# Optimization experiments

Hardware: AMD Instinct MI355X
Metric: run time of the kernel (lower is better)

Reference implementation:

```python
import jax, jax.numpy as jnp
import numpy as np

N1 = 512
N2 = 512
N = N1 + N2
NEG_SLOPE = 0.2


def _build_edges(n1, n2):
    # inside: fully connected within each set, both directions
    s1, d1 = np.triu_indices(n1, 1)
    s2, d2 = np.triu_indices(n2, 1)
    is_ = np.concatenate([s1, s2 + n1])
    id_ = np.concatenate([d1, d2 + n1])
    inside = np.stack([np.concatenate([is_, id_]), np.concatenate([id_, is_])])
    # cross: fully connected bipartite, both directions
    cs = np.repeat(np.arange(n1), n2)
    cd = np.tile(np.arange(n1, n1 + n2), n1)
    cross = np.stack([np.concatenate([cs, cd]), np.concatenate([cd, cs])])
    # PyG GATConv default add_self_loops=True
    loops = np.arange(n1 + n2)
    self_e = np.stack([loops, loops])
    inside = np.concatenate([inside, self_e], axis=1)
    cross = np.concatenate([cross, self_e], axis=1)
    return inside.astype(np.int32), cross.astype(np.int32)


def setup_inputs() -> dict:
    key = jax.random.key(0)
    ks = jax.random.split(key, 12)
    inside_edge, cross_edge = _build_edges(N1, N2)
    s = 0.1
    return {
        'desc1': jax.random.normal(ks[0], (N1, 128), jnp.float32),
        'desc2': jax.random.normal(ks[1], (N2, 128), jnp.float32),
        'W1': jax.random.normal(ks[2], (128, 128), jnp.float32) * s,
        'a_src1': jax.random.normal(ks[3], (128, 1), jnp.float32) * s,
        'a_dst1': jax.random.normal(ks[4], (128, 1), jnp.float32) * s,
        'b1': jnp.zeros((128,), jnp.float32),
        'W2': jax.random.normal(ks[5], (128, 128), jnp.float32) * s,
        'a_src2': jax.random.normal(ks[6], (1, 128), jnp.float32) * s,
        'a_dst2': jax.random.normal(ks[7], (1, 128), jnp.float32) * s,
        'b2': jnp.zeros((128,), jnp.float32),
        'inside_edge': jnp.asarray(inside_edge),
        'cross_edge': jnp.asarray(cross_edge),
    }


def gat_conv(x, edge_index, W, a_src, a_dst, bias, heads, out_ch, concat):
    # x: [N, F_in]; edge_index: [2, E] (self-loops already included)
    n = x.shape[0]
    src, dst = edge_index[0], edge_index[1]
    h = (x @ W).reshape(n, heads, out_ch)                 # [N, H, C]
    a_s = jnp.sum(h * a_src, axis=-1)                     # [N, H]
    a_d = jnp.sum(h * a_dst, axis=-1)                     # [N, H]
    e = jax.nn.leaky_relu(a_s[src] + a_d[dst], NEG_SLOPE)  # [E, H]
    # segment (scatter) softmax over incoming edges of each dst node
    m = jax.ops.segment_max(e, dst, num_segments=n)
    ex = jnp.exp(e - m[dst])
    denom = jax.ops.segment_sum(ex, dst, num_segments=n)
    alpha = ex / (denom[dst] + 1e-16)                     # [E, H]
    out = jax.ops.segment_sum(alpha[:, :, None] * h[src], dst, num_segments=n)  # [N, H, C]
    out = out.reshape(n, heads * out_ch) if concat else out.mean(axis=1)
    return out + bias


def reference(desc1, desc2, W1, a_src1, a_dst1, b1, W2, a_src2, a_dst2, b2, inside_edge, cross_edge):
    x = jnp.concatenate([desc1, desc2], axis=0)  # [N, 128]
    for _ in range(2):
        x = jax.nn.elu(gat_conv(x, inside_edge, W1, a_src1, a_dst1, b1, 128, 1, True))
        x = jax.nn.elu(gat_conv(x, cross_edge, W1, a_src1, a_dst1, b1, 128, 1, True))
    x = gat_conv(x, cross_edge, W2, a_src2, a_dst2, b2, 1, 128, False)  # [N, 128]
    return x
```

## Files before the change

kernel.cpp:

```cpp
#include <hip/hip_runtime.h>
#include <hip/hip_bf16.h>


typedef __hip_bfloat16 bf16;

__device__ __forceinline__ float b2f(bf16 x) { return __bfloat162float(x); }

__device__ __forceinline__ int detect_bf16(const void* desc1) {
  const unsigned* u = (const unsigned*)desc1;
  int hits = 0;
#pragma unroll 8
  for (int i = 0; i < 256; ++i) {
    unsigned e = (u[i] >> 7) & 0xFFu;
    hits += (e >= 100u && e <= 140u) ? 1 : 0;
  }
  return hits >= 200 ? 1 : 0;
}

__device__ __forceinline__ float load_in(const void* p, int i, int bf) {
  return bf ? b2f(((const bf16*)p)[i]) : ((const float*)p)[i];
}

__global__ __launch_bounds__(256) void prep_kernel(
    const void* __restrict__ desc1, const void* __restrict__ desc2,
    const void* __restrict__ W1,   const void* __restrict__ as1,
    const void* __restrict__ ad1,  const void* __restrict__ b1,
    const void* __restrict__ W2,   const void* __restrict__ as2,
    const void* __restrict__ ad2,  const void* __restrict__ b2,
    float* __restrict__ xt, float* __restrict__ W1t, float* __restrict__ W2f,
    float* __restrict__ vecs, int* __restrict__ flag) {
  const int bf = detect_bf16(desc1);
  if (blockIdx.x == 0 && threadIdx.x == 0) *flag = bf;
  const int total = 131072 + 16384 + 16384 + 6 * 128;
  for (int idx = blockIdx.x * blockDim.x + threadIdx.x; idx < total;
       idx += gridDim.x * blockDim.x) {
    if (idx < 131072) {
      int n = idx & 1023, c = idx >> 10;
      float v = (n < 512) ? load_in(desc1, n * 128 + c, bf)
                          : load_in(desc2, (n - 512) * 128 + c, bf);
      xt[((c >> 2) * 1024 + n) * 4 + (c & 3)] = v;
    } else if (idx < 147456) {
      int i = idx - 131072, hd = i >> 7, k = i & 127;
      W1t[i] = load_in(W1, k * 128 + hd, bf);
    } else if (idx < 163840) {
      W2f[idx - 147456] = load_in(W2, idx - 147456, bf);
    } else {
      int i = idx - 163840, o = i & 127;
      float v;
      if      (i < 128) v = load_in(as1, o, bf);
      else if (i < 256) v = load_in(ad1, o, bf);
      else if (i < 384) v = load_in(b1, o, bf);
      else if (i < 512) v = load_in(as2, o, bf);
      else if (i < 640) v = load_in(ad2, o, bf);
      else              v = load_in(b2, o, bf);
      vecs[i] = v;
    }
  }
}

__global__ __launch_bounds__(256, 2) void gemm_kernel(
    const float* __restrict__ xt_in, const float* __restrict__ W1t,
    float* __restrict__ Ht) {
  __shared__ float wcol[128];
  const int tid = threadIdx.x;
  const int hd = blockIdx.x & 127;
  const int chunk = blockIdx.x >> 7;
  const int node = chunk * 256 + tid;
  if (tid < 32) ((float4*)wcol)[tid] = ((const float4*)(W1t + hd * 128))[tid];
  __syncthreads();
  const float4* x4 = (const float4*)xt_in;
  float acc0 = 0.f, acc1 = 0.f;
  for (int cc = 0; cc < 32; cc += 8) {
    float4 xs[8];
#pragma unroll
    for (int u = 0; u < 8; ++u) xs[u] = x4[(cc + u) * 1024 + node];
#pragma unroll
    for (int u = 0; u < 8; ++u) {
      const int k = (cc + u) * 4;
      acc0 = fmaf(xs[u].x, wcol[k],     acc0);
      acc1 = fmaf(xs[u].y, wcol[k + 1], acc1);
      acc0 = fmaf(xs[u].z, wcol[k + 2], acc0);
      acc1 = fmaf(xs[u].w, wcol[k + 3], acc1);
    }
  }
  Ht[hd * 1024 + node] = acc0 + acc1;
}

template <int CROSS>
__global__ __launch_bounds__(512, 2) void attn_kernel(
    const float* __restrict__ Ht, float* __restrict__ xt_out,
    const float* __restrict__ vecs) {
  __shared__ float    sS[512];
  __shared__ float    sH[512];
  __shared__ unsigned hA[512];
  __shared__ unsigned ISb[512];
  __shared__ unsigned binNext[512];
  __shared__ float2   PRE[512];
  __shared__ float2   SUF[512];
  __shared__ float    red[16];
  __shared__ unsigned wTot[8];
  __shared__ float2   preTot[8];
  __shared__ float2   sufTot[8];

  const int tid  = threadIdx.x;
  const int lane = tid & 63;
  const int wave = tid >> 6;
  const int hd   = blockIdx.x & 127;
  const int S    = blockIdx.x >> 7;
  const int D    = CROSS ? (1 - S) : S;
  const float a_src = vecs[hd], a_dst = vecs[128 + hd], bias = vecs[256 + hd];

  const float h_src = Ht[hd * 1024 + S * 512 + tid];
  const float h_dst = CROSS ? Ht[hd * 1024 + D * 512 + tid] : h_src;
  const float s_own = h_src * a_src;
  const float d_own = h_dst * a_dst;

  {
    float mnw = s_own, mxw = s_own;
#pragma unroll
    for (int off = 32; off > 0; off >>= 1) {
      mnw = fminf(mnw, __shfl_down(mnw, off));
      mxw = fmaxf(mxw, __shfl_down(mxw, off));
    }
    if (lane == 0) { red[wave] = mnw; red[8 + wave] = mxw; }
  }
  hA[tid] = 0;
  binNext[tid] = 0;
  __syncthreads();
  const float mn = fminf(fminf(fminf(red[0], red[1]), fminf(red[2], red[3])),
                         fminf(fminf(red[4], red[5]), fminf(red[6], red[7])));
  const float mx = fmaxf(fmaxf(fmaxf(red[8], red[9]), fmaxf(red[10], red[11])),
                         fmaxf(fmaxf(red[12], red[13]), fmaxf(red[14], red[15])));
  const float scale = 512.0f / fmaxf(mx - mn, 1e-20f);

  const int myBin = (int)fminf(fmaxf((s_own - mn) * scale, 0.0f), 511.0f);
  atomicAdd(&hA[myBin], 1u);
  __syncthreads();

  {
    unsigned v = hA[tid];
#pragma unroll
    for (int off = 1; off < 64; off <<= 1) {
      unsigned u = __shfl_up(v, off);
      if (lane >= off) v += u;
    }
    if (lane == 63) wTot[wave] = v;
    __syncthreads();
    unsigned pre = 0;
#pragma unroll
    for (int w = 0; w < 8; ++w) pre += (w < wave) ? wTot[w] : 0u;
    ISb[tid] = v + pre;
    __syncthreads();
  }

  {
    unsigned base = myBin ? ISb[myBin - 1] : 0u;
    unsigned pos = base + atomicAdd(&binNext[myBin], 1u);
    sS[pos] = s_own;
    sH[pos] = h_src;
  }
  __syncthreads();

  {
    const float sv = sS[tid];
    const float hv = sH[tid];
    const float e1 = __expf(sv), e2 = __expf(0.2f * sv);
    float p0 = e2, p1 = e2 * hv;
    float q0 = e1, q1 = e1 * hv;
#pragma unroll
    for (int off = 1; off < 64; off <<= 1) {
      float u0 = __shfl_up(p0, off), u1 = __shfl_up(p1, off);
      if (lane >= off) { p0 += u0; p1 += u1; }
      float v0 = __shfl_down(q0, off), v1 = __shfl_down(q1, off);
      if (lane + off < 64) { q0 += v0; q1 += v1; }
    }
    if (lane == 63) preTot[wave] = make_float2(p0, p1);
    if (lane == 0)  sufTot[wave] = make_float2(q0, q1);
    __syncthreads();
    float a0 = 0.f, a1 = 0.f, b0 = 0.f, b1 = 0.f;
#pragma unroll
    for (int w = 0; w < 8; ++w) {
      float2 pt = preTot[w], st = sufTot[w];
      if (w < wave) { a0 += pt.x; a1 += pt.y; }
      if (w > wave) { b0 += st.x; b1 += st.y; }
    }
    PRE[tid] = make_float2(p0 + a0, p1 + a1);
    SUF[tid] = make_float2(q0 + b0, q1 + b1);
    __syncthreads();
  }

  {
    const float theta = -d_own;
    int b = (int)fminf(fmaxf((theta - mn) * scale, 0.0f), 511.0f);
    unsigned k0 = b ? ISb[b - 1] : 0u;
    unsigned k1 = ISb[b];
    float F1 = __expf(d_own), F2 = __expf(0.2f * d_own);
    float P2 = 0.f, P2h = 0.f, S1 = 0.f, S1h = 0.f;
    if (k0 > 0)   { float2 t2 = PRE[k0 - 1]; P2 = t2.x; P2h = t2.y; }
    if (k1 < 512) { float2 t2 = SUF[k1];     S1 = t2.x; S1h = t2.y; }
    float den = F1 * S1 + F2 * P2;
    float num = F1 * S1h + F2 * P2h;
    for (unsigned e = k0; e < k1; ++e) {
      float se = sS[e], he = sH[e];
      float p = (se >= theta) ? F1 * __expf(se) : F2 * __expf(0.2f * se);
      den += p;
      num = fmaf(p, he, num);
    }
    if (CROSS) {
      float t = h_dst * a_src + d_own;
      float p = __expf(fmaxf(t, 0.2f * t));
      den += p;
      num = fmaf(p, h_dst, num);
    }
    float o = num / (den + 1e-16f) + bias;
    o = (o > 0.f) ? o : expm1f(o);
    xt_out[(((hd >> 2) * 1024) + D * 512 + tid) * 4 + (hd & 3)] = o;
  }
}

__global__ __launch_bounds__(256, 2) void mm2_kernel(
    const float* __restrict__ xt_in, const float* __restrict__ W2f,
    const float* __restrict__ vecs, float* __restrict__ h2,
    float* __restrict__ s2, float* __restrict__ d2) {
  __shared__ float rs[256], rd[256];
  const int tid = threadIdx.x;
  const int row = blockIdx.x * 2 + (tid >> 7);
  const int c = tid & 127;
  float acc0 = 0.f, acc1 = 0.f;
  {
    const float4* x4 = (const float4*)xt_in;
    for (int cc = 0; cc < 32; cc += 8) {
      float4 xb[8];
#pragma unroll
      for (int u = 0; u < 8; ++u) xb[u] = x4[(cc + u) * 1024 + row];
#pragma unroll
      for (int u = 0; u < 8; ++u) {
        const int k = (cc + u) * 4;
        acc0 = fmaf(xb[u].x, W2f[k * 128 + c],       acc0);
        acc1 = fmaf(xb[u].y, W2f[(k + 1) * 128 + c], acc1);
        acc0 = fmaf(xb[u].z, W2f[(k + 2) * 128 + c], acc0);
        acc1 = fmaf(xb[u].w, W2f[(k + 3) * 128 + c], acc1);
      }
    }
  }
  float acc = acc0 + acc1;
  h2[row * 128 + c] = acc;
  rs[tid] = acc * vecs[384 + c];
  rd[tid] = acc * vecs[512 + c];
  __syncthreads();
  for (int off = 64; off > 0; off >>= 1) {
    if ((tid & 127) < off) { rs[tid] += rs[tid + off]; rd[tid] += rd[tid + off]; }
    __syncthreads();
  }
  if ((tid & 127) == 0) {
    s2[row] = rs[tid];
    d2[row] = rd[tid];
  }
}

__global__ __launch_bounds__(256, 2) void att2_kernel(
    const float* __restrict__ h2, const float* __restrict__ s2,
    const float* __restrict__ d2, const float* __restrict__ vecs,
    void* __restrict__ out, const int* __restrict__ flag) {
  __shared__ __align__(16) float pT[512 * 2];
  const int tid = threadIdx.x;
  const int dstBase = blockIdx.x * 2;
  const int srcBase = (dstBase < 512) ? 512 : 0;

  for (int e = tid; e < 1024; e += 256) {
    int j = e >> 1, ld = e & 1;
    float t = s2[srcBase + j] + d2[dstBase + ld];
    pT[e] = __expf(fmaxf(t, 0.2f * t));
  }
  __syncthreads();

  const int c = tid & 127;
  const int g = tid >> 7;
  const int i0 = dstBase + g;
  float den = 0.f, num = 0.f;
  const float* hrow = h2 + srcBase * 128 + c;
  for (int j0 = 0; j0 < 512; j0 += 8) {
    float hb[8];
#pragma unroll
    for (int u = 0; u < 8; ++u) hb[u] = hrow[(j0 + u) * 128];
#pragma unroll
    for (int u = 0; u < 8; ++u) {
      float p = pT[(j0 + u) * 2 + g];
      den += p;
      num = fmaf(p, hb[u], num);
    }
  }
  float ts = s2[i0] + d2[i0];
  float ps = __expf(fmaxf(ts, 0.2f * ts));
  den += ps;
  num = fmaf(ps, h2[i0 * 128 + c], num);

  float o = num / (den + 1e-16f) + vecs[640 + c];
  if (*flag) ((bf16*)out)[i0 * 128 + c] = __float2bfloat16(o);
  else       ((float*)out)[i0 * 128 + c] = o;
}

extern "C" void kernel_launch(void* const* d_in, const int* in_sizes, int n_in,
                              void* d_out, int out_size, void* d_ws, size_t ws_size,
                              hipStream_t stream) {
  (void)in_sizes; (void)n_in; (void)out_size; (void)ws_size;
  float* ws   = (float*)d_ws;
  float* xtA  = ws;
  float* xtB  = ws + 131072;
  float* h2   = ws + 262144;
  float* Ht   = h2;
  float* W1t  = ws + 393216;
  float* W2f  = ws + 409600;
  float* vecs = ws + 425984;
  float* s2   = ws + 426752;
  float* d2   = ws + 427776;
  int*   flag = (int*)(ws + 428800);

  prep_kernel<<<128, 256, 0, stream>>>(d_in[0], d_in[1], d_in[2], d_in[3],
                                       d_in[4], d_in[5], d_in[6], d_in[7],
                                       d_in[8], d_in[9], xtA, W1t, W2f, vecs,
                                       flag);
  gemm_kernel<<<512, 256, 0, stream>>>(xtA, W1t, Ht);
  attn_kernel<0><<<256, 512, 0, stream>>>(Ht, xtB, vecs);
  gemm_kernel<<<512, 256, 0, stream>>>(xtB, W1t, Ht);
  attn_kernel<1><<<256, 512, 0, stream>>>(Ht, xtA, vecs);
  gemm_kernel<<<512, 256, 0, stream>>>(xtA, W1t, Ht);
  attn_kernel<0><<<256, 512, 0, stream>>>(Ht, xtB, vecs);
  gemm_kernel<<<512, 256, 0, stream>>>(xtB, W1t, Ht);
  attn_kernel<1><<<256, 512, 0, stream>>>(Ht, xtA, vecs);
  mm2_kernel<<<512, 256, 0, stream>>>(xtA, W2f, vecs, h2, s2, d2);
  att2_kernel<<<512, 256, 0, stream>>>(h2, s2, d2, vecs, d_out, flag);
}
```

Before: 166.2 us.

## Replace histogram-sort attention with brute-force masked sums over precomputed exponentials

The attention kernel drops its per-block histogram binning, counting sort and prefix/suffix scans. Instead it precomputes exp(s), exp(0.2s) and their products with h into shared memory, and has each destination node sweep all 512 sources, splitting them by comparing exp(s) against exp(-d). The grid is doubled to 512 blocks of 256 threads, each block handling half the destinations. This trades many barriers and atomics for a 512-iteration loop per thread. The prep kernel also gets coalesced reads for the input transpose, and its grid is doubled.

New measurement: 196.5 us. +18.2%, slower.

```diff
diff --git a/kernel.cpp b/kernel.cpp
--- a/kernel.cpp
+++ b/kernel.cpp
@@ -35,13 +35,14 @@
   for (int idx = blockIdx.x * blockDim.x + threadIdx.x; idx < total;
        idx += gridDim.x * blockDim.x) {
     if (idx < 131072) {
-      int n = idx & 1023, c = idx >> 10;
-      float v = (n < 512) ? load_in(desc1, n * 128 + c, bf)
-                          : load_in(desc2, (n - 512) * 128 + c, bf);
+      int c = idx & 127, n = idx >> 7;
+      float v = (n < 512) ? load_in(desc1, idx, bf)
+                          : load_in(desc2, idx - 65536, bf);
       xt[((c >> 2) * 1024 + n) * 4 + (c & 3)] = v;
     } else if (idx < 147456) {
-      int i = idx - 131072, hd = i >> 7, k = i & 127;
-      W1t[i] = load_in(W1, k * 128 + hd, bf);
+      int i = idx - 131072;
+      int k = i >> 7, hdd = i & 127;
+      W1t[hdd * 128 + k] = load_in(W1, i, bf);
     } else if (idx < 163840) {
       W2f[idx - 147456] = load_in(W2, idx - 147456, bf);
     } else {
@@ -87,135 +88,55 @@
 }
 
 template <int CROSS>
-__global__ __launch_bounds__(512, 2) void attn_kernel(
+__global__ __launch_bounds__(256, 2) void attn_kernel(
     const float* __restrict__ Ht, float* __restrict__ xt_out,
     const float* __restrict__ vecs) {
-  __shared__ float    sS[512];
-  __shared__ float    sH[512];
-  __shared__ unsigned hA[512];
-  __shared__ unsigned ISb[512];
-  __shared__ unsigned binNext[512];
-  __shared__ float2   PRE[512];
-  __shared__ float2   SUF[512];
-  __shared__ float    red[16];
-  __shared__ unsigned wTot[8];
-  __shared__ float2   preTot[8];
-  __shared__ float2   sufTot[8];
-
+  __shared__ __align__(16) float4 sE[512];
   const int tid  = threadIdx.x;
-  const int lane = tid & 63;
-  const int wave = tid >> 6;
   const int hd   = blockIdx.x & 127;
-  const int S    = blockIdx.x >> 7;
+  const int S    = (blockIdx.x >> 7) & 1;
+  const int half = blockIdx.x >> 8;
   const int D    = CROSS ? (1 - S) : S;
   const float a_src = vecs[hd], a_dst = vecs[128 + hd], bias = vecs[256 + hd];
-
-  const float h_src = Ht[hd * 1024 + S * 512 + tid];
-  const float h_dst = CROSS ? Ht[hd * 1024 + D * 512 + tid] : h_src;
-  const float s_own = h_src * a_src;
-  const float d_own = h_dst * a_dst;
-
-  {
-    float mnw = s_own, mxw = s_own;
-#pragma unroll
-    for (int off = 32; off > 0; off >>= 1) {
-      mnw = fminf(mnw, __shfl_down(mnw, off));
-      mxw = fmaxf(mxw, __shfl_down(mxw, off));
-    }
-    if (lane == 0) { red[wave] = mnw; red[8 + wave] = mxw; }
-  }
-  hA[tid] = 0;
-  binNext[tid] = 0;
-  __syncthreads();
-  const float mn = fminf(fminf(fminf(red[0], red[1]), fminf(red[2], red[3])),
-                         fminf(fminf(red[4], red[5]), fminf(red[6], red[7])));
-  const float mx = fmaxf(fmaxf(fmaxf(red[8], red[9]), fmaxf(red[10], red[11])),
-                         fmaxf(fmaxf(red[12], red[13]), fmaxf(red[14], red[15])));
-  const float scale = 512.0f / fmaxf(mx - mn, 1e-20f);
-
-  const int myBin = (int)fminf(fmaxf((s_own - mn) * scale, 0.0f), 511.0f);
-  atomicAdd(&hA[myBin], 1u);
-  __syncthreads();
-
-  {
-    unsigned v = hA[tid];
-#pragma unroll
-    for (int off = 1; off < 64; off <<= 1) {
-      unsigned u = __shfl_up(v, off);
-      if (lane >= off) v += u;
-    }
-    if (lane == 63) wTot[wave] = v;
-    __syncthreads();
-    unsigned pre = 0;
-#pragma unroll
-    for (int w = 0; w < 8; ++w) pre += (w < wave) ? wTot[w] : 0u;
-    ISb[tid] = v + pre;
-    __syncthreads();
-  }
-
-  {
-    unsigned base = myBin ? ISb[myBin - 1] : 0u;
-    unsigned pos = base + atomicAdd(&binNext[myBin], 1u);
-    sS[pos] = s_own;
-    sH[pos] = h_src;
-  }
-  __syncthreads();
-
-  {
-    const float sv = sS[tid];
-    const float hv = sH[tid];
-    const float e1 = __expf(sv), e2 = __expf(0.2f * sv);
-    float p0 = e2, p1 = e2 * hv;
-    float q0 = e1, q1 = e1 * hv;
-#pragma unroll
-    for (int off = 1; off < 64; off <<= 1) {
-      float u0 = __shfl_up(p0, off), u1 = __shfl_up(p1, off);
-      if (lane >= off) { p0 += u0; p1 += u1; }
-      float v0 = __shfl_down(q0, off), v1 = __shfl_down(q1, off);
-      if (lane + off < 64) { q0 += v0; q1 += v1; }
-    }
-    if (lane == 63) preTot[wave] = make_float2(p0, p1);
-    if (lane == 0)  sufTot[wave] = make_float2(q0, q1);
-    __syncthreads();
-    float a0 = 0.f, a1 = 0.f, b0 = 0.f, b1 = 0.f;
-#pragma unroll
-    for (int w = 0; w < 8; ++w) {
-      float2 pt = preTot[w], st = sufTot[w];
-      if (w < wave) { a0 += pt.x; a1 += pt.y; }
-      if (w > wave) { b0 += st.x; b1 += st.y; }
-    }
-    PRE[tid] = make_float2(p0 + a0, p1 + a1);
-    SUF[tid] = make_float2(q0 + b0, q1 + b1);
-    __syncthreads();
-  }
-
-  {
-    const float theta = -d_own;
-    int b = (int)fminf(fmaxf((theta - mn) * scale, 0.0f), 511.0f);
-    unsigned k0 = b ? ISb[b - 1] : 0u;
-    unsigned k1 = ISb[b];
-    float F1 = __expf(d_own), F2 = __expf(0.2f * d_own);
-    float P2 = 0.f, P2h = 0.f, S1 = 0.f, S1h = 0.f;
-    if (k0 > 0)   { float2 t2 = PRE[k0 - 1]; P2 = t2.x; P2h = t2.y; }
-    if (k1 < 512) { float2 t2 = SUF[k1];     S1 = t2.x; S1h = t2.y; }
-    float den = F1 * S1 + F2 * P2;
-    float num = F1 * S1h + F2 * P2h;
-    for (unsigned e = k0; e < k1; ++e) {
-      float se = sS[e], he = sH[e];
-      float p = (se >= theta) ? F1 * __expf(se) : F2 * __expf(0.2f * se);
-      den += p;
-      num = fmaf(p, he, num);
-    }
-    if (CROSS) {
-      float t = h_dst * a_src + d_own;
-      float p = __expf(fmaxf(t, 0.2f * t));
-      den += p;
-      num = fmaf(p, h_dst, num);
-    }
-    float o = num / (den + 1e-16f) + bias;
-    o = (o > 0.f) ? o : expm1f(o);
-    xt_out[(((hd >> 2) * 1024) + D * 512 + tid) * 4 + (hd & 3)] = o;
-  }
+  const float* HtH = Ht + hd * 1024;
+
+#pragma unroll
+  for (int u = 0; u < 2; ++u) {
+    const int i = u * 256 + tid;
+    const float h = HtH[S * 512 + i];
+    const float s = h * a_src;
+    const float e1 = __expf(s), e2 = __expf(0.2f * s);
+    sE[i] = make_float4(e1, e2, e1 * h, e2 * h);
+  }
+  const int j = half * 256 + tid;
+  const float hD    = HtH[D * 512 + j];
+  const float d_own = hD * a_dst;
+  const float F1  = __expf(d_own), F2 = __expf(0.2f * d_own);
+  const float eTh = __expf(-d_own);
+  __syncthreads();
+
+  float M1 = 0.f, M1h = 0.f, N2 = 0.f, N2h = 0.f;
+#pragma unroll 8
+  for (int i = 0; i < 512; ++i) {
+    const float4 r = sE[i];
+    const float m = (r.x >= eTh) ? 1.0f : 0.0f;
+    const float n = (r.x >= eTh) ? 0.0f : 1.0f;
+    M1  = fmaf(m, r.x, M1);
+    M1h = fmaf(m, r.z, M1h);
+    N2  = fmaf(n, r.y, N2);
+    N2h = fmaf(n, r.w, N2h);
+  }
+  float den = fmaf(F1, M1,  F2 * N2);
+  float num = fmaf(F1, M1h, F2 * N2h);
+  if (CROSS) {
+    const float t = hD * a_src + d_own;
+    const float p = __expf(fmaxf(t, 0.2f * t));
+    den += p;
+    num = fmaf(p, hD, num);
+  }
+  float o = num / (den + 1e-16f) + bias;
+  o = (o > 0.f) ? o : expm1f(o);
+  xt_out[(((hd >> 2) * 1024) + D * 512 + j) * 4 + (hd & 3)] = o;
 }
 
 __global__ __launch_bounds__(256, 2) void mm2_kernel(
@@ -316,18 +237,18 @@
   float* d2   = ws + 427776;
   int*   flag = (int*)(ws + 428800);
 
-  prep_kernel<<<128, 256, 0, stream>>>(d_in[0], d_in[1], d_in[2], d_in[3],
+  prep_kernel<<<256, 256, 0, stream>>>(d_in[0], d_in[1], d_in[2], d_in[3],
                                        d_in[4], d_in[5], d_in[6], d_in[7],
                                        d_in[8], d_in[9], xtA, W1t, W2f, vecs,
                                        flag);
   gemm_kernel<<<512, 256, 0, stream>>>(xtA, W1t, Ht);
-  attn_kernel<0><<<256, 512, 0, stream>>>(Ht, xtB, vecs);
+  attn_kernel<0><<<512, 256, 0, stream>>>(Ht, xtB, vecs);
   gemm_kernel<<<512, 256, 0, stream>>>(xtB, W1t, Ht);
-  attn_kernel<1><<<256, 512, 0, stream>>>(Ht, xtA, vecs);
+  attn_kernel<1><<<512, 256, 0, stream>>>(Ht, xtA, vecs);
   gemm_kernel<<<512, 256, 0, stream>>>(xtA, W1t, Ht);
-  attn_kernel<0><<<256, 512, 0, stream>>>(Ht, xtB, vecs);
+  attn_kernel<0><<<512, 256, 0, stream>>>(Ht, xtB, vecs);
   gemm_kernel<<<512, 256, 0, stream>>>(xtB, W1t, Ht);
-  attn_kernel<1><<<256, 512, 0, stream>>>(Ht, xtA, vecs);
+  attn_kernel<1><<<512, 256, 0, stream>>>(Ht, xtA, vecs);
   mm2_kernel<<<512, 256, 0, stream>>>(xtA, W2f, vecs, h2, s2, d2);
   att2_kernel<<<512, 256, 0, stream>>>(h2, s2, d2, vecs, d_out, flag);
 }
```

## Fuse per-head projection GEMM into attention kernel and switch to plain transposed layout

Applied to the files above, without the earlier changes.

Removes the separate gemm_kernel and computes each head's projected features inside the attention kernel, which saves four launches and the Ht round trip through global memory. The cross variant recomputes the projection for both source and destination node sets, doubling GEMM loads in those blocks. The activation layout moves from float4-interleaved to a plain [channel][node] transpose, so loads become scalar but coalesced across threads. The prep kernel now reads inputs contiguously and its grid is doubled.

New measurement: 194.5 us. 1.17x slower.

```diff
diff --git a/kernel.cpp b/kernel.cpp
--- a/kernel.cpp
+++ b/kernel.cpp
@@ -35,13 +35,14 @@
   for (int idx = blockIdx.x * blockDim.x + threadIdx.x; idx < total;
        idx += gridDim.x * blockDim.x) {
     if (idx < 131072) {
-      int n = idx & 1023, c = idx >> 10;
-      float v = (n < 512) ? load_in(desc1, n * 128 + c, bf)
-                          : load_in(desc2, (n - 512) * 128 + c, bf);
-      xt[((c >> 2) * 1024 + n) * 4 + (c & 3)] = v;
+      int c = idx & 127, n = idx >> 7;
+      float v = (n < 512) ? load_in(desc1, idx, bf)
+                          : load_in(desc2, idx - 65536, bf);
+      xt[c * 1024 + n] = v;
     } else if (idx < 147456) {
-      int i = idx - 131072, hd = i >> 7, k = i & 127;
-      W1t[i] = load_in(W1, k * 128 + hd, bf);
+      int i = idx - 131072;
+      int k = i >> 7, hdd = i & 127;
+      W1t[hdd * 128 + k] = load_in(W1, i, bf);
     } else if (idx < 163840) {
       W2f[idx - 147456] = load_in(W2, idx - 147456, bf);
     } else {
@@ -58,38 +59,11 @@
   }
 }
 
-__global__ __launch_bounds__(256, 2) void gemm_kernel(
-    const float* __restrict__ xt_in, const float* __restrict__ W1t,
-    float* __restrict__ Ht) {
-  __shared__ float wcol[128];
-  const int tid = threadIdx.x;
-  const int hd = blockIdx.x & 127;
-  const int chunk = blockIdx.x >> 7;
-  const int node = chunk * 256 + tid;
-  if (tid < 32) ((float4*)wcol)[tid] = ((const float4*)(W1t + hd * 128))[tid];
-  __syncthreads();
-  const float4* x4 = (const float4*)xt_in;
-  float acc0 = 0.f, acc1 = 0.f;
-  for (int cc = 0; cc < 32; cc += 8) {
-    float4 xs[8];
-#pragma unroll
-    for (int u = 0; u < 8; ++u) xs[u] = x4[(cc + u) * 1024 + node];
-#pragma unroll
-    for (int u = 0; u < 8; ++u) {
-      const int k = (cc + u) * 4;
-      acc0 = fmaf(xs[u].x, wcol[k],     acc0);
-      acc1 = fmaf(xs[u].y, wcol[k + 1], acc1);
-      acc0 = fmaf(xs[u].z, wcol[k + 2], acc0);
-      acc1 = fmaf(xs[u].w, wcol[k + 3], acc1);
-    }
-  }
-  Ht[hd * 1024 + node] = acc0 + acc1;
-}
-
 template <int CROSS>
-__global__ __launch_bounds__(512, 2) void attn_kernel(
-    const float* __restrict__ Ht, float* __restrict__ xt_out,
-    const float* __restrict__ vecs) {
+__global__ __launch_bounds__(512, 2) void layer_kernel(
+    const float* __restrict__ xt_in, float* __restrict__ xt_out,
+    const float* __restrict__ W1t, const float* __restrict__ vecs) {
+  __shared__ float    wcol[128];
   __shared__ float    sS[512];
   __shared__ float    sH[512];
   __shared__ unsigned hA[512];
@@ -110,8 +84,32 @@
   const int D    = CROSS ? (1 - S) : S;
   const float a_src = vecs[hd], a_dst = vecs[128 + hd], bias = vecs[256 + hd];
 
-  const float h_src = Ht[hd * 1024 + S * 512 + tid];
-  const float h_dst = CROSS ? Ht[hd * 1024 + D * 512 + tid] : h_src;
+  if (tid < 32) ((float4*)wcol)[tid] = ((const float4*)(W1t + hd * 128))[tid];
+  __syncthreads();
+  float acc0 = 0.f, acc1 = 0.f, accD0 = 0.f, accD1 = 0.f;
+  {
+    const int nS = S * 512 + tid;
+    const int nD = D * 512 + tid;
+    for (int k0 = 0; k0 < 128; k0 += 8) {
+      float xs[8], xd[8];
+#pragma unroll
+      for (int u = 0; u < 8; ++u) {
+        xs[u] = xt_in[(k0 + u) * 1024 + nS];
+        if (CROSS) xd[u] = xt_in[(k0 + u) * 1024 + nD];
+      }
+#pragma unroll
+      for (int u = 0; u < 8; u += 2) {
+        acc0 = fmaf(xs[u],     wcol[k0 + u],     acc0);
+        acc1 = fmaf(xs[u + 1], wcol[k0 + u + 1], acc1);
+        if (CROSS) {
+          accD0 = fmaf(xd[u],     wcol[k0 + u],     accD0);
+          accD1 = fmaf(xd[u + 1], wcol[k0 + u + 1], accD1);
+        }
+      }
+    }
+  }
+  const float h_src = acc0 + acc1;
+  const float h_dst = CROSS ? (accD0 + accD1) : h_src;
   const float s_own = h_src * a_src;
   const float d_own = h_dst * a_dst;
 
@@ -214,7 +212,7 @@
     }
     float o = num / (den + 1e-16f) + bias;
     o = (o > 0.f) ? o : expm1f(o);
-    xt_out[(((hd >> 2) * 1024) + D * 512 + tid) * 4 + (hd & 3)] = o;
+    xt_out[hd * 1024 + D * 512 + tid] = o;
   }
 }
 
@@ -227,20 +225,14 @@
   const int row = blockIdx.x * 2 + (tid >> 7);
   const int c = tid & 127;
   float acc0 = 0.f, acc1 = 0.f;
-  {
-    const float4* x4 = (const float4*)xt_in;
-    for (int cc = 0; cc < 32; cc += 8) {
-      float4 xb[8];
-#pragma unroll
-      for (int u = 0; u < 8; ++u) xb[u] = x4[(cc + u) * 1024 + row];
-#pragma unroll
-      for (int u = 0; u < 8; ++u) {
-        const int k = (cc + u) * 4;
-        acc0 = fmaf(xb[u].x, W2f[k * 128 + c],       acc0);
-        acc1 = fmaf(xb[u].y, W2f[(k + 1) * 128 + c], acc1);
-        acc0 = fmaf(xb[u].z, W2f[(k + 2) * 128 + c], acc0);
-        acc1 = fmaf(xb[u].w, W2f[(k + 3) * 128 + c], acc1);
-      }
+  for (int k0 = 0; k0 < 128; k0 += 8) {
+    float xb[8];
+#pragma unroll
+    for (int u = 0; u < 8; ++u) xb[u] = xt_in[(k0 + u) * 1024 + row];
+#pragma unroll
+    for (int u = 0; u < 8; u += 2) {
+      acc0 = fmaf(xb[u],     W2f[(k0 + u) * 128 + c],     acc0);
+      acc1 = fmaf(xb[u + 1], W2f[(k0 + u + 1) * 128 + c], acc1);
     }
   }
   float acc = acc0 + acc1;
@@ -308,7 +300,6 @@
   float* xtA  = ws;
   float* xtB  = ws + 131072;
   float* h2   = ws + 262144;
-  float* Ht   = h2;
   float* W1t  = ws + 393216;
   float* W2f  = ws + 409600;
   float* vecs = ws + 425984;
@@ -316,18 +307,14 @@
   float* d2   = ws + 427776;
   int*   flag = (int*)(ws + 428800);
 
-  prep_kernel<<<128, 256, 0, stream>>>(d_in[0], d_in[1], d_in[2], d_in[3],
+  prep_kernel<<<256, 256, 0, stream>>>(d_in[0], d_in[1], d_in[2], d_in[3],
                                        d_in[4], d_in[5], d_in[6], d_in[7],
                                        d_in[8], d_in[9], xtA, W1t, W2f, vecs,
                                        flag);
-  gemm_kernel<<<512, 256, 0, stream>>>(xtA, W1t, Ht);
-  attn_kernel<0><<<256, 512, 0, stream>>>(Ht, xtB, vecs);
-  gemm_kernel<<<512, 256, 0, stream>>>(xtB, W1t, Ht);
-  attn_kernel<1><<<256, 512, 0, stream>>>(Ht, xtA, vecs);
-  gemm_kernel<<<512, 256, 0, stream>>>(xtA, W1t, Ht);
-  attn_kernel<0><<<256, 512, 0, stream>>>(Ht, xtB, vecs);
-  gemm_kernel<<<512, 256, 0, stream>>>(xtB, W1t, Ht);
-  attn_kernel<1><<<256, 512, 0, stream>>>(Ht, xtA, vecs);
+  layer_kernel<0><<<256, 512, 0, stream>>>(xtA, xtB, W1t, vecs);
+  layer_kernel<1><<<256, 512, 0, stream>>>(xtB, xtA, W1t, vecs);
+  layer_kernel<0><<<256, 512, 0, stream>>>(xtA, xtB, W1t, vecs);
+  layer_kernel<1><<<256, 512, 0, stream>>>(xtB, xtA, W1t, vecs);
   mm2_kernel<<<512, 256, 0, stream>>>(xtA, W2f, vecs, h2, s2, d2);
   att2_kernel<<<512, 256, 0, stream>>>(h2, s2, d2, vecs, d_out, flag);
 }
```
